# Kernel optimization log

Measured on AMD Instinct MI355X. Metric: run time of the kernel, lower is better.

Reference implementation:

```python
import jax, jax.numpy as jnp
import numpy as np

N, E = 10000, 320000
IN, H, C, ED = 256, 4, 64, 64
HC = H * C
EPS = 1e-5
NEG_SLOPE = 0.2


def setup_inputs() -> dict:
    key = jax.random.key(0)
    ks = jax.random.split(key, 12)
    g = lambda k, shape, fan: jax.random.normal(k, shape, jnp.float32) * (1.0 / np.sqrt(fan))
    return {
        "x": jax.random.normal(ks[0], (N, IN), jnp.float32),
        "edge_index": jax.random.randint(ks[1], (2, E), 0, N, jnp.int64),
        "edge_attr": jax.random.normal(ks[2], (E, ED), jnp.float32),
        "Wl": g(ks[3], (HC, IN), IN),   # lin_l weight (source)
        "bl": jnp.zeros((HC,), jnp.float32),
        "Wr": g(ks[4], (HC, IN), IN),   # lin_r weight (target)
        "br": jnp.zeros((HC,), jnp.float32),
        "We": g(ks[5], (HC, ED), ED),   # lin_edge weight (no bias)
        "att": g(ks[6], (H, C), C),
        "bias": jnp.zeros((HC,), jnp.float32),
        "gamma": jnp.ones((HC,), jnp.float32),
        "beta": jnp.zeros((HC,), jnp.float32),
    }


def reference(x, edge_index, edge_attr, Wl, bl, Wr, br, We, att, bias, gamma, beta):
    src, dst = edge_index[0], edge_index[1]
    # add_self_loops with fill_value='mean': loop edge_attr = mean of incoming attrs
    ones = jnp.ones((E,), jnp.float32)
    cnt = jax.ops.segment_sum(ones, dst, num_segments=N)              # [N]
    loop_attr = jax.ops.segment_sum(edge_attr, dst, num_segments=N) / jnp.maximum(cnt, 1.0)[:, None]
    node_ids = jnp.arange(N, dtype=src.dtype)
    src_f = jnp.concatenate([src, node_ids])                          # [E+N]
    dst_f = jnp.concatenate([dst, node_ids])
    ea = jnp.concatenate([edge_attr, loop_attr], axis=0)              # [E+N, ED]

    xl = (x @ Wl.T + bl).reshape(N, H, C)   # source-side projection
    xr = (x @ Wr.T + br).reshape(N, H, C)   # target-side projection
    ep = (ea @ We.T).reshape(-1, H, C)       # edge projection

    m = xl[src_f] + xr[dst_f] + ep                                    # [E+N, H, C]
    m = jnp.where(m >= 0, m, NEG_SLOPE * m)                           # leaky_relu(0.2)
    logits = jnp.einsum("ehc,hc->eh", m, att)                        # [E+N, H]

    # segment softmax over target node dst_f (every node has a self loop)
    mx = jax.ops.segment_max(logits, dst_f, num_segments=N)
    ex = jnp.exp(logits - mx[dst_f])
    den = jax.ops.segment_sum(ex, dst_f, num_segments=N)
    alpha = ex / den[dst_f]                                           # [E+N, H]

    out = jax.ops.segment_sum(xl[src_f] * alpha[:, :, None], dst_f, num_segments=N)
    h = out.reshape(N, HC) + bias

    # SiLU then LayerNorm, dropout is identity in eval
    h = h * jax.nn.sigmoid(h)
    mu = jnp.mean(h, axis=-1, keepdims=True)
    var = jnp.mean((h - mu) ** 2, axis=-1, keepdims=True)
    h = (h - mu) * jax.lax.rsqrt(var + EPS) * gamma + beta
    return h, alpha
```

## Files before the change

kernel.cpp:

```cpp
#include <hip/hip_runtime.h>

#define N_NODES 10000
#define N_EDGES 320000
#define NE_TOT  330000
#define NEG_SLOPE 0.2f
#define LN_EPS 1e-5f

#define OFF_CNT    0u
#define OFF_FILL   40000u
#define OFF_ROWPTR 80128u
#define OFF_EIDS   120320u
#define OFF_LATTR  1440512u
#define OFF_XLH    4000512u
#define OFF_XRH    9120512u
#define OFF_LOG    14240512u
#define OFF_WLF    19520512u
#define OFF_WRF    19651584u

typedef __bf16 bf16x8 __attribute__((ext_vector_type(8)));
typedef float  f32x4  __attribute__((ext_vector_type(4)));
typedef unsigned short us4 __attribute__((ext_vector_type(4)));

__device__ __forceinline__ float bf2f(unsigned short u) {
    union { unsigned int i; float f; } v;
    v.i = ((unsigned int)u) << 16;
    return v.f;
}
__device__ __forceinline__ unsigned short f2bf(float x) {
    __bf16 b = (__bf16)x;
    return __builtin_bit_cast(unsigned short, b);
}
__device__ __forceinline__ bf16x8 cvt8(const float* p) {
    float4 v0 = *reinterpret_cast<const float4*>(p);
    float4 v1 = *reinterpret_cast<const float4*>(p + 4);
    bf16x8 t;
    t[0] = (__bf16)v0.x; t[1] = (__bf16)v0.y; t[2] = (__bf16)v0.z; t[3] = (__bf16)v0.w;
    t[4] = (__bf16)v1.x; t[5] = (__bf16)v1.y; t[6] = (__bf16)v1.z; t[7] = (__bf16)v1.w;
    return t;
}

__global__ void k_count(const int* __restrict__ ei, int* __restrict__ cnt) {
    int e = blockIdx.x * blockDim.x + threadIdx.x;
    if (e < N_EDGES) atomicAdd(&cnt[ei[N_EDGES + e]], 1);
}

__global__ void k_scan(const int* __restrict__ cnt, int* __restrict__ row_ptr) {
    __shared__ int sums[1024];
    int t = threadIdx.x;
    const int CH = 10;
    int base = t * CH;
    int s = 0;
    for (int i = 0; i < CH; i++) {
        int n = base + i;
        if (n < N_NODES) s += cnt[n] + 1;
    }
    sums[t] = s;
    __syncthreads();
    for (int off = 1; off < 1024; off <<= 1) {
        int v = (t >= off) ? sums[t - off] : 0;
        __syncthreads();
        sums[t] += v;
        __syncthreads();
    }
    int run = (t == 0) ? 0 : sums[t - 1];
    for (int i = 0; i < CH; i++) {
        int n = base + i;
        if (n < N_NODES) { row_ptr[n] = run; run += cnt[n] + 1; }
    }
    if (t == 1023) row_ptr[N_NODES] = sums[1023];
}

__global__ void k_fill(const int* __restrict__ ei, const int* __restrict__ row_ptr,
                       int* __restrict__ fill, int* __restrict__ eids) {
    int e = blockIdx.x * blockDim.x + threadIdx.x;
    if (e >= NE_TOT) return;
    int d = (e < N_EDGES) ? ei[N_EDGES + e] : (e - N_EDGES);
    int pos = atomicAdd(&fill[d], 1);
    eids[row_ptr[d] + pos] = e;
}

__global__ void k_loop_attr(const float* __restrict__ edge_attr,
                            const int* __restrict__ row_ptr,
                            const int* __restrict__ eids,
                            const int* __restrict__ cnt,
                            float* __restrict__ lattr) {
    int node = (blockIdx.x << 2) + (threadIdx.x >> 6);
    int lane = threadIdx.x & 63;
    int b = row_ptr[node], en = row_ptr[node + 1];
    float s0 = 0.0f, s1 = 0.0f, s2 = 0.0f, s3 = 0.0f;
    int i = b;
    for (; i + 3 < en; i += 4) {
        int e0 = eids[i], e1 = eids[i + 1], e2 = eids[i + 2], e3 = eids[i + 3];
        int v0 = e0 < N_EDGES, v1 = e1 < N_EDGES, v2 = e2 < N_EDGES, v3 = e3 < N_EDGES;
        float a0 = edge_attr[(size_t)(v0 ? e0 : 0) * 64 + lane];
        float a1 = edge_attr[(size_t)(v1 ? e1 : 0) * 64 + lane];
        float a2 = edge_attr[(size_t)(v2 ? e2 : 0) * 64 + lane];
        float a3 = edge_attr[(size_t)(v3 ? e3 : 0) * 64 + lane];
        s0 += v0 ? a0 : 0.0f;
        s1 += v1 ? a1 : 0.0f;
        s2 += v2 ? a2 : 0.0f;
        s3 += v3 ? a3 : 0.0f;
    }
    for (; i < en; i++) {
        int e = eids[i];
        int v = e < N_EDGES;
        float a = edge_attr[(size_t)(v ? e : 0) * 64 + lane];
        s0 += v ? a : 0.0f;
    }
    float s = (s0 + s1) + (s2 + s3);
    float c = (float)cnt[node];
    lattr[node * 64 + lane] = s / fmaxf(c, 1.0f);
}

__global__ void k_prep_wfrag(const float* __restrict__ Wl,
                             const float* __restrict__ Wr,
                             unsigned short* __restrict__ wlf,
                             unsigned short* __restrict__ wrf) {
    int idx = blockIdx.x * 256 + threadIdx.x;
    if (idx >= 8192) return;
    int ln = idx & 63;
    int ts = (idx >> 6) & 7;
    int ct = idx >> 9;
    int c = ct * 16 + (ln & 15);
    int k0 = ts * 32 + (ln >> 4) * 8;
    *reinterpret_cast<bf16x8*>(wlf + (size_t)idx * 8) = cvt8(Wl + (size_t)c * 256 + k0);
    *reinterpret_cast<bf16x8*>(wrf + (size_t)idx * 8) = cvt8(Wr + (size_t)c * 256 + k0);
}

__global__ __launch_bounds__(256) void k_gemm_mfma(
        const float* __restrict__ x,
        const float* __restrict__ bl, const float* __restrict__ br,
        const unsigned short* __restrict__ wlf,
        const unsigned short* __restrict__ wrf,
        unsigned short* __restrict__ xlh,
        unsigned short* __restrict__ xrh) {
    __shared__ __bf16 xs[8 * 64 * 8];
    int tid = threadIdx.x;
    int nb = blockIdx.x * 16;

    for (int f = tid; f < 512; f += 256) {
        int t = f >> 6, ln = f & 63;
        int node = nb + (ln & 15);
        int k0 = t * 32 + (ln >> 4) * 8;
        *reinterpret_cast<bf16x8*>(&xs[f * 8]) = cvt8(x + (size_t)node * 256 + k0);
    }
    __syncthreads();

    int lane = tid & 63;
    int wv = tid >> 6;
    int quad = lane >> 4;
    int ln15 = lane & 15;

    bf16x8 bfr[8];
#pragma unroll
    for (int t = 0; t < 8; t++)
        bfr[t] = *reinterpret_cast<const bf16x8*>(&xs[(t * 64 + lane) * 8]);

    int node = nb + ln15;
#pragma unroll
    for (int ci = 0; ci < 4; ci++) {
        int ct = wv * 4 + ci;
        f32x4 accl, accr;
        accl[0] = accl[1] = accl[2] = accl[3] = 0.0f;
        accr[0] = accr[1] = accr[2] = accr[3] = 0.0f;
#pragma unroll
        for (int t = 0; t < 8; t++) {
            bf16x8 al = *reinterpret_cast<const bf16x8*>(
                wlf + ((size_t)(ct * 8 + t) * 64 + lane) * 8);
            accl = __builtin_amdgcn_mfma_f32_16x16x32_bf16(al, bfr[t], accl, 0, 0, 0);
        }
#pragma unroll
        for (int t = 0; t < 8; t++) {
            bf16x8 ar = *reinterpret_cast<const bf16x8*>(
                wrf + ((size_t)(ct * 8 + t) * 64 + lane) * 8);
            accr = __builtin_amdgcn_mfma_f32_16x16x32_bf16(ar, bfr[t], accr, 0, 0, 0);
        }
        int cbase = ct * 16 + quad * 4;
        float4 blv = *reinterpret_cast<const float4*>(bl + cbase);
        float4 brv = *reinterpret_cast<const float4*>(br + cbase);
        us4 ol, orr;
        ol[0] = f2bf(accl[0] + blv.x); ol[1] = f2bf(accl[1] + blv.y);
        ol[2] = f2bf(accl[2] + blv.z); ol[3] = f2bf(accl[3] + blv.w);
        orr[0] = f2bf(accr[0] + brv.x); orr[1] = f2bf(accr[1] + brv.y);
        orr[2] = f2bf(accr[2] + brv.z); orr[3] = f2bf(accr[3] + brv.w);
        *reinterpret_cast<us4*>(xlh + (size_t)node * 256 + cbase) = ol;
        *reinterpret_cast<us4*>(xrh + (size_t)node * 256 + cbase) = orr;
    }
}

__global__ __launch_bounds__(256) void k_logits_mfma(
        const int* __restrict__ ei,
        const int* __restrict__ eids,
        const float* __restrict__ edge_attr,
        const float* __restrict__ lattr,
        const unsigned short* __restrict__ xlh,
        const unsigned short* __restrict__ xrh,
        const float* __restrict__ We, const float* __restrict__ att,
        float* __restrict__ logits) {
    __shared__ __bf16 fb[32 * 64 * 8];
    __shared__ float att_s[256];
    int tid = threadIdx.x;

    for (int idx = tid; idx < 2048; idx += 256) {
        int f = idx >> 6, ls = idx & 63;
        int cb = f >> 1, step = f & 1;
        int c = cb * 16 + (ls & 15);
        int k = step * 32 + (ls >> 4) * 8;
        *reinterpret_cast<bf16x8*>(&fb[idx * 8]) = cvt8(We + (size_t)c * 64 + k);
    }
    if (tid < 64) {
        reinterpret_cast<float4*>(att_s)[tid] =
            reinterpret_cast<const float4*>(att)[tid];
    }
    __syncthreads();

    int lane = tid & 63;
    int wv = tid >> 6;
    int quad = lane >> 4;
    int ln15 = lane & 15;

    const int ntiles = NE_TOT / 16;
    for (int t = blockIdx.x * 4 + wv; t < ntiles; t += gridDim.x * 4) {
        int pos = t * 16 + ln15;
        int e = eids[pos];
        int s, d;
        const float* row;
        if (e < N_EDGES) {
            s = ei[e]; d = ei[N_EDGES + e];
            row = edge_attr + (size_t)e * 64;
        } else {
            s = e - N_EDGES; d = s;
            row = lattr + (size_t)(e - N_EDGES) * 64;
        }

        bf16x8 bfr[2];
#pragma unroll
        for (int step = 0; step < 2; step++)
            bfr[step] = cvt8(row + step * 32 + quad * 8);

        const unsigned short* xls = xlh + (size_t)s * 256;
        const unsigned short* xrd = xrh + (size_t)d * 256;

        float hsum[4] = {0.0f, 0.0f, 0.0f, 0.0f};
#pragma unroll 4
        for (int cb = 0; cb < 16; cb++) {
            f32x4 acc;
            acc[0] = acc[1] = acc[2] = acc[3] = 0.0f;
            bf16x8 a0 = *reinterpret_cast<const bf16x8*>(&fb[((cb * 2 + 0) * 64 + lane) * 8]);
            bf16x8 a1 = *reinterpret_cast<const bf16x8*>(&fb[((cb * 2 + 1) * 64 + lane) * 8]);
            acc = __builtin_amdgcn_mfma_f32_16x16x32_bf16(a0, bfr[0], acc, 0, 0, 0);
            acc = __builtin_amdgcn_mfma_f32_16x16x32_bf16(a1, bfr[1], acc, 0, 0, 0);

            int cbase = cb * 16 + quad * 4;
            us4 xa = *reinterpret_cast<const us4*>(xls + cbase);
            us4 xb = *reinterpret_cast<const us4*>(xrd + cbase);
            float4 at = *reinterpret_cast<const float4*>(&att_s[cbase]);
            const float* tp = reinterpret_cast<const float*>(&at);
            float hs = 0.0f;
#pragma unroll
            for (int r = 0; r < 4; r++) {
                float v = acc[r] + bf2f(xa[r]) + bf2f(xb[r]);
                v = (v >= 0.0f) ? v : NEG_SLOPE * v;
                hs = fmaf(v, tp[r], hs);
            }
            hsum[cb >> 2] += hs;
        }
#pragma unroll
        for (int hh = 0; hh < 4; hh++) {
            hsum[hh] += __shfl_xor(hsum[hh], 16, 64);
            hsum[hh] += __shfl_xor(hsum[hh], 32, 64);
        }
        if (quad == 0) {
            reinterpret_cast<float4*>(logits)[pos] =
                make_float4(hsum[0], hsum[1], hsum[2], hsum[3]);
        }
    }
}

__global__ void k_aggregate(const int* __restrict__ ei,
                            const int* __restrict__ row_ptr,
                            const int* __restrict__ eids,
                            const float* __restrict__ logits,
                            const unsigned short* __restrict__ xlh,
                            const float* __restrict__ bias,
                            const float* __restrict__ gamma,
                            const float* __restrict__ beta,
                            float* __restrict__ hout,
                            float* __restrict__ alpha_out) {
    int node = (blockIdx.x << 2) + (threadIdx.x >> 6);
    int lane = threadIdx.x & 63;
    int h = lane >> 4;
    int b = row_ptr[node], en = row_ptr[node + 1];

    float m0 = -INFINITY, m1 = -INFINITY, m2 = -INFINITY, m3 = -INFINITY;
    int i = b;
    for (; i + 3 < en; i += 4) {
        m0 = fmaxf(m0, logits[(i + 0) * 4 + h]);
        m1 = fmaxf(m1, logits[(i + 1) * 4 + h]);
        m2 = fmaxf(m2, logits[(i + 2) * 4 + h]);
        m3 = fmaxf(m3, logits[(i + 3) * 4 + h]);
    }
    for (; i < en; i++) m0 = fmaxf(m0, logits[i * 4 + h]);
    float mh = fmaxf(fmaxf(m0, m1), fmaxf(m2, m3));

    float d0 = 0.0f, d1 = 0.0f, d2 = 0.0f, d3 = 0.0f;
    i = b;
    for (; i + 3 < en; i += 4) {
        d0 += __expf(logits[(i + 0) * 4 + h] - mh);
        d1 += __expf(logits[(i + 1) * 4 + h] - mh);
        d2 += __expf(logits[(i + 2) * 4 + h] - mh);
        d3 += __expf(logits[(i + 3) * 4 + h] - mh);
    }
    for (; i < en; i++) d0 += __expf(logits[i * 4 + h] - mh);
    float rden = 1.0f / ((d0 + d1) + (d2 + d3));

    int c0 = lane * 4;
    float4 ac0; ac0.x = ac0.y = ac0.z = ac0.w = 0.0f;
    float4 ac1; ac1.x = ac1.y = ac1.z = ac1.w = 0.0f;
    float4 ac2; ac2.x = ac2.y = ac2.z = ac2.w = 0.0f;
    float4 ac3; ac3.x = ac3.y = ac3.z = ac3.w = 0.0f;
    i = b;
    for (; i + 3 < en; i += 4) {
        int e0 = eids[i], e1 = eids[i + 1], e2 = eids[i + 2], e3 = eids[i + 3];
        float al0 = __expf(logits[(i + 0) * 4 + h] - mh) * rden;
        float al1 = __expf(logits[(i + 1) * 4 + h] - mh) * rden;
        float al2 = __expf(logits[(i + 2) * 4 + h] - mh) * rden;
        float al3 = __expf(logits[(i + 3) * 4 + h] - mh) * rden;
        if ((lane & 15) == 0) {
            alpha_out[e0 * 4 + h] = al0;
            alpha_out[e1 * 4 + h] = al1;
            alpha_out[e2 * 4 + h] = al2;
            alpha_out[e3 * 4 + h] = al3;
        }
        int s0 = (e0 < N_EDGES) ? ei[e0] : (e0 - N_EDGES);
        int s1 = (e1 < N_EDGES) ? ei[e1] : (e1 - N_EDGES);
        int s2 = (e2 < N_EDGES) ? ei[e2] : (e2 - N_EDGES);
        int s3 = (e3 < N_EDGES) ? ei[e3] : (e3 - N_EDGES);
        us4 x0 = *reinterpret_cast<const us4*>(xlh + (size_t)s0 * 256 + c0);
        us4 x1 = *reinterpret_cast<const us4*>(xlh + (size_t)s1 * 256 + c0);
        us4 x2 = *reinterpret_cast<const us4*>(xlh + (size_t)s2 * 256 + c0);
        us4 x3 = *reinterpret_cast<const us4*>(xlh + (size_t)s3 * 256 + c0);
        ac0.x = fmaf(al0, bf2f(x0[0]), ac0.x); ac0.y = fmaf(al0, bf2f(x0[1]), ac0.y);
        ac0.z = fmaf(al0, bf2f(x0[2]), ac0.z); ac0.w = fmaf(al0, bf2f(x0[3]), ac0.w);
        ac1.x = fmaf(al1, bf2f(x1[0]), ac1.x); ac1.y = fmaf(al1, bf2f(x1[1]), ac1.y);
        ac1.z = fmaf(al1, bf2f(x1[2]), ac1.z); ac1.w = fmaf(al1, bf2f(x1[3]), ac1.w);
        ac2.x = fmaf(al2, bf2f(x2[0]), ac2.x); ac2.y = fmaf(al2, bf2f(x2[1]), ac2.y);
        ac2.z = fmaf(al2, bf2f(x2[2]), ac2.z); ac2.w = fmaf(al2, bf2f(x2[3]), ac2.w);
        ac3.x = fmaf(al3, bf2f(x3[0]), ac3.x); ac3.y = fmaf(al3, bf2f(x3[1]), ac3.y);
        ac3.z = fmaf(al3, bf2f(x3[2]), ac3.z); ac3.w = fmaf(al3, bf2f(x3[3]), ac3.w);
    }
    for (; i < en; i++) {
        int e = eids[i];
        float al = __expf(logits[i * 4 + h] - mh) * rden;
        if ((lane & 15) == 0) alpha_out[e * 4 + h] = al;
        int s = (e < N_EDGES) ? ei[e] : (e - N_EDGES);
        us4 xv = *reinterpret_cast<const us4*>(xlh + (size_t)s * 256 + c0);
        ac0.x = fmaf(al, bf2f(xv[0]), ac0.x); ac0.y = fmaf(al, bf2f(xv[1]), ac0.y);
        ac0.z = fmaf(al, bf2f(xv[2]), ac0.z); ac0.w = fmaf(al, bf2f(xv[3]), ac0.w);
    }
    float4 acc;
    acc.x = (ac0.x + ac1.x) + (ac2.x + ac3.x);
    acc.y = (ac0.y + ac1.y) + (ac2.y + ac3.y);
    acc.z = (ac0.z + ac1.z) + (ac2.z + ac3.z);
    acc.w = (ac0.w + ac1.w) + (ac2.w + ac3.w);

    const float4 b4 = reinterpret_cast<const float4*>(bias)[lane];
    float4 hv;
    hv.x = acc.x + b4.x; hv.y = acc.y + b4.y;
    hv.z = acc.z + b4.z; hv.w = acc.w + b4.w;
    hv.x = hv.x / (1.0f + __expf(-hv.x));
    hv.y = hv.y / (1.0f + __expf(-hv.y));
    hv.z = hv.z / (1.0f + __expf(-hv.z));
    hv.w = hv.w / (1.0f + __expf(-hv.w));
    float s1 = hv.x + hv.y + hv.z + hv.w;
    float s2 = hv.x * hv.x + hv.y * hv.y + hv.z * hv.z + hv.w * hv.w;
#pragma unroll
    for (int off = 1; off < 64; off <<= 1) {
        s1 += __shfl_xor(s1, off, 64);
        s2 += __shfl_xor(s2, off, 64);
    }
    float mu = s1 * (1.0f / 256.0f);
    float var = s2 * (1.0f / 256.0f) - mu * mu;
    float rs = rsqrtf(var + LN_EPS);
    const float4 g4 = reinterpret_cast<const float4*>(gamma)[lane];
    const float4 be4 = reinterpret_cast<const float4*>(beta)[lane];
    float4 o;
    o.x = (hv.x - mu) * rs * g4.x + be4.x;
    o.y = (hv.y - mu) * rs * g4.y + be4.y;
    o.z = (hv.z - mu) * rs * g4.z + be4.z;
    o.w = (hv.w - mu) * rs * g4.w + be4.w;
    reinterpret_cast<float4*>(hout)[node * 64 + lane] = o;
}

extern "C" void kernel_launch(void* const* d_in, const int* in_sizes, int n_in,
                              void* d_out, int out_size, void* d_ws, size_t ws_size,
                              hipStream_t stream) {
    (void)in_sizes; (void)n_in; (void)out_size; (void)ws_size;
    const float* x         = (const float*)d_in[0];
    const int*   ei        = (const int*)d_in[1];
    const float* edge_attr = (const float*)d_in[2];
    const float* Wl        = (const float*)d_in[3];
    const float* bl        = (const float*)d_in[4];
    const float* Wr        = (const float*)d_in[5];
    const float* br        = (const float*)d_in[6];
    const float* We        = (const float*)d_in[7];
    const float* att       = (const float*)d_in[8];
    const float* bias      = (const float*)d_in[9];
    const float* gamma     = (const float*)d_in[10];
    const float* beta      = (const float*)d_in[11];

    char* ws = (char*)d_ws;
    int*   cnt     = (int*)(ws + OFF_CNT);
    int*   fill    = (int*)(ws + OFF_FILL);
    int*   row_ptr = (int*)(ws + OFF_ROWPTR);
    int*   eids    = (int*)(ws + OFF_EIDS);
    float* lattr   = (float*)(ws + OFF_LATTR);
    unsigned short* xlh = (unsigned short*)(ws + OFF_XLH);
    unsigned short* xrh = (unsigned short*)(ws + OFF_XRH);
    float* logits  = (float*)(ws + OFF_LOG);
    unsigned short* wlf = (unsigned short*)(ws + OFF_WLF);
    unsigned short* wrf = (unsigned short*)(ws + OFF_WRF);

    float* hout      = (float*)d_out;
    float* alpha_out = (float*)d_out + N_NODES * 256;

    hipMemsetAsync(ws + OFF_CNT, 0, 2 * N_NODES * sizeof(int), stream);

    k_count<<<(N_EDGES + 255) / 256, 256, 0, stream>>>(ei, cnt);
    k_scan<<<1, 1024, 0, stream>>>(cnt, row_ptr);
    k_prep_wfrag<<<32, 256, 0, stream>>>(Wl, Wr, wlf, wrf);
    k_fill<<<(NE_TOT + 255) / 256, 256, 0, stream>>>(ei, row_ptr, fill, eids);
    k_gemm_mfma<<<N_NODES / 16, 256, 0, stream>>>(x, bl, br, wlf, wrf, xlh, xrh);
    k_loop_attr<<<N_NODES / 4, 256, 0, stream>>>(edge_attr, row_ptr, eids, cnt, lattr);
    k_logits_mfma<<<2579, 256, 0, stream>>>(ei, eids, edge_attr, lattr, xlh, xrh,
                                            We, att, logits);
    k_aggregate<<<N_NODES / 4, 256, 0, stream>>>(ei, row_ptr, eids, logits, xlh,
                                                 bias, gamma, beta, hout, alpha_out);
}
```

Before: 379.4 us.

## Store per-edge src/dst in CSR order and pre-permute edge attrs to bf16

During CSR fill, the source and destination of each edge are written in sorted order, along with an inverse permutation. When the workspace is large enough, edge attributes are scattered into CSR order as bf16 and the self-loop mean is computed in place. The logits kernel can then read src, dst and attributes contiguously instead of gathering through eids and ei. This adds a scatter pass and extra workspace traffic, and the self-loop mean is now averaged from bf16-rounded attributes.

```diff
diff --git a/kernel.cpp b/kernel.cpp
--- a/kernel.cpp
+++ b/kernel.cpp
@@ -9,17 +9,23 @@
 #define OFF_CNT    0u
 #define OFF_FILL   40000u
 #define OFF_ROWPTR 80128u
-#define OFF_EIDS   120320u
-#define OFF_LATTR  1440512u
-#define OFF_XLH    4000512u
-#define OFF_XRH    9120512u
-#define OFF_LOG    14240512u
-#define OFF_WLF    19520512u
-#define OFF_WRF    19651584u
+#define OFF_EIDS   120192u
+#define OFF_SRCS   1440192u
+#define OFF_DSTS   2760192u
+#define OFF_LATTR  4080192u
+#define OFF_XLH    6640192u
+#define OFF_XRH    11760192u
+#define OFF_LOG    16880192u
+#define OFF_WLF    22160192u
+#define OFF_WRF    22291264u
+#define OFF_INV    22422336u
+#define OFF_EAP    23742336u
+#define WS_NEED_A  65982336u
 
 typedef __bf16 bf16x8 __attribute__((ext_vector_type(8)));
 typedef float  f32x4  __attribute__((ext_vector_type(4)));
 typedef unsigned short us4 __attribute__((ext_vector_type(4)));
+typedef unsigned short us8 __attribute__((ext_vector_type(8)));
 
 __device__ __forceinline__ float bf2f(unsigned short u) {
     union { unsigned int i; float f; } v;
@@ -71,18 +77,54 @@
 }
 
 __global__ void k_fill(const int* __restrict__ ei, const int* __restrict__ row_ptr,
-                       int* __restrict__ fill, int* __restrict__ eids) {
+                       int* __restrict__ fill, int* __restrict__ eids,
+                       int* __restrict__ srcs, int* __restrict__ dsts,
+                       int* __restrict__ inv) {
     int e = blockIdx.x * blockDim.x + threadIdx.x;
     if (e >= NE_TOT) return;
-    int d = (e < N_EDGES) ? ei[N_EDGES + e] : (e - N_EDGES);
+    int s, d;
+    if (e < N_EDGES) { s = ei[e]; d = ei[N_EDGES + e]; }
+    else             { s = e - N_EDGES; d = s; }
     int pos = atomicAdd(&fill[d], 1);
-    eids[row_ptr[d] + pos] = e;
+    int p = row_ptr[d] + pos;
+    eids[p] = e;
+    srcs[p] = s;
+    dsts[p] = d;
+    inv[e] = p;
+}
+
+__global__ void k_perm_ea(const float* __restrict__ edge_attr,
+                          const int* __restrict__ inv,
+                          unsigned short* __restrict__ eap) {
+    int e = blockIdx.x * 4 + (threadIdx.x >> 6);
+    int lane = threadIdx.x & 63;
+    if (e >= N_EDGES) return;
+    float v = edge_attr[(size_t)e * 64 + lane];
+    eap[(size_t)inv[e] * 64 + lane] = f2bf(v);
+}
+
+__global__ void k_selfmean(const int* __restrict__ row_ptr,
+                           const int* __restrict__ eids,
+                           unsigned short* __restrict__ eap) {
+    int node = (blockIdx.x << 2) + (threadIdx.x >> 6);
+    int lane = threadIdx.x & 63;
+    int b = row_ptr[node], en = row_ptr[node + 1];
+    float s = 0.0f;
+    int selfpos = b;
+    for (int i = b; i < en; i++) {
+        int e = eids[i];
+        bool real = (e < N_EDGES);
+        unsigned short u = eap[(size_t)i * 64 + lane];
+        s += real ? bf2f(u) : 0.0f;
+        selfpos = real ? selfpos : i;
+    }
+    float c = (float)(en - b - 1);
+    eap[(size_t)selfpos * 64 + lane] = f2bf(s / fmaxf(c, 1.0f));
 }
 
 __global__ void k_loop_attr(const float* __restrict__ edge_attr,
                             const int* __restrict__ row_ptr,
                             const int* __restrict__ eids,
-                            const int* __restrict__ cnt,
                             float* __restrict__ lattr) {
     int node = (blockIdx.x << 2) + (threadIdx.x >> 6);
     int lane = threadIdx.x & 63;
@@ -108,7 +150,7 @@
         s0 += v ? a : 0.0f;
     }
     float s = (s0 + s1) + (s2 + s3);
-    float c = (float)cnt[node];
+    float c = (float)(en - b - 1);
     lattr[node * 64 + lane] = s / fmaxf(c, 1.0f);
 }
 
@@ -188,8 +230,10 @@
     }
 }
 
+template <bool USE_EAP>
 __global__ __launch_bounds__(256) void k_logits_mfma(
-        const int* __restrict__ ei,
+        const int* __restrict__ srcs, const int* __restrict__ dsts,
+        const unsigned short* __restrict__ eap,
         const int* __restrict__ eids,
         const float* __restrict__ edge_attr,
         const float* __restrict__ lattr,
@@ -222,21 +266,22 @@
     const int ntiles = NE_TOT / 16;
     for (int t = blockIdx.x * 4 + wv; t < ntiles; t += gridDim.x * 4) {
         int pos = t * 16 + ln15;
-        int e = eids[pos];
-        int s, d;
-        const float* row;
-        if (e < N_EDGES) {
-            s = ei[e]; d = ei[N_EDGES + e];
-            row = edge_attr + (size_t)e * 64;
+        int s = srcs[pos];
+        int d = dsts[pos];
+
+        bf16x8 bfr[2];
+        if (USE_EAP) {
+            const unsigned short* er = eap + (size_t)pos * 64 + quad * 8;
+            bfr[0] = __builtin_bit_cast(bf16x8, *reinterpret_cast<const us8*>(er));
+            bfr[1] = __builtin_bit_cast(bf16x8, *reinterpret_cast<const us8*>(er + 32));
         } else {
-            s = e - N_EDGES; d = s;
-            row = lattr + (size_t)(e - N_EDGES) * 64;
-        }
-
-        bf16x8 bfr[2];
-#pragma unroll
-        for (int step = 0; step < 2; step++)
-            bfr[step] = cvt8(row + step * 32 + quad * 8);
+            int e = eids[pos];
+            const float* row = (e < N_EDGES)
+                ? edge_attr + (size_t)e * 64
+                : lattr + (size_t)(e - N_EDGES) * 64;
+            bfr[0] = cvt8(row + quad * 8);
+            bfr[1] = cvt8(row + 32 + quad * 8);
+        }
 
         const unsigned short* xls = xlh + (size_t)s * 256;
         const unsigned short* xrd = xrh + (size_t)d * 256;
@@ -277,9 +322,9 @@
     }
 }
 
-__global__ void k_aggregate(const int* __restrict__ ei,
-                            const int* __restrict__ row_ptr,
+__global__ void k_aggregate(const int* __restrict__ row_ptr,
                             const int* __restrict__ eids,
+                            const int* __restrict__ srcs,
                             const float* __restrict__ logits,
                             const unsigned short* __restrict__ xlh,
                             const float* __restrict__ bias,
@@ -322,6 +367,7 @@
     i = b;
     for (; i + 3 < en; i += 4) {
         int e0 = eids[i], e1 = eids[i + 1], e2 = eids[i + 2], e3 = eids[i + 3];
+        int s0 = srcs[i], s1 = srcs[i + 1], s2 = srcs[i + 2], s3 = srcs[i + 3];
         float al0 = __expf(logits[(i + 0) * 4 + h] - mh) * rden;
         float al1 = __expf(logits[(i + 1) * 4 + h] - mh) * rden;
         float al2 = __expf(logits[(i + 2) * 4 + h] - mh) * rden;
@@ -332,10 +378,6 @@
             alpha_out[e2 * 4 + h] = al2;
             alpha_out[e3 * 4 + h] = al3;
         }
-        int s0 = (e0 < N_EDGES) ? ei[e0] : (e0 - N_EDGES);
-        int s1 = (e1 < N_EDGES) ? ei[e1] : (e1 - N_EDGES);
-        int s2 = (e2 < N_EDGES) ? ei[e2] : (e2 - N_EDGES);
-        int s3 = (e3 < N_EDGES) ? ei[e3] : (e3 - N_EDGES);
         us4 x0 = *reinterpret_cast<const us4*>(xlh + (size_t)s0 * 256 + c0);
         us4 x1 = *reinterpret_cast<const us4*>(xlh + (size_t)s1 * 256 + c0);
         us4 x2 = *reinterpret_cast<const us4*>(xlh + (size_t)s2 * 256 + c0);
@@ -351,9 +393,9 @@
     }
     for (; i < en; i++) {
         int e = eids[i];
+        int s = srcs[i];
         float al = __expf(logits[i * 4 + h] - mh) * rden;
         if ((lane & 15) == 0) alpha_out[e * 4 + h] = al;
-        int s = (e < N_EDGES) ? ei[e] : (e - N_EDGES);
         us4 xv = *reinterpret_cast<const us4*>(xlh + (size_t)s * 256 + c0);
         ac0.x = fmaf(al, bf2f(xv[0]), ac0.x); ac0.y = fmaf(al, bf2f(xv[1]), ac0.y);
         ac0.z = fmaf(al, bf2f(xv[2]), ac0.z); ac0.w = fmaf(al, bf2f(xv[3]), ac0.w);
@@ -395,7 +437,7 @@
 extern "C" void kernel_launch(void* const* d_in, const int* in_sizes, int n_in,
                               void* d_out, int out_size, void* d_ws, size_t ws_size,
                               hipStream_t stream) {
-    (void)in_sizes; (void)n_in; (void)out_size; (void)ws_size;
+    (void)in_sizes; (void)n_in; (void)out_size;
     const float* x         = (const float*)d_in[0];
     const int*   ei        = (const int*)d_in[1];
     const float* edge_attr = (const float*)d_in[2];
@@ -414,26 +456,42 @@
     int*   fill    = (int*)(ws + OFF_FILL);
     int*   row_ptr = (int*)(ws + OFF_ROWPTR);
     int*   eids    = (int*)(ws + OFF_EIDS);
+    int*   srcs    = (int*)(ws + OFF_SRCS);
+    int*   dsts    = (int*)(ws + OFF_DSTS);
     float* lattr   = (float*)(ws + OFF_LATTR);
     unsigned short* xlh = (unsigned short*)(ws + OFF_XLH);
     unsigned short* xrh = (unsigned short*)(ws + OFF_XRH);
     float* logits  = (float*)(ws + OFF_LOG);
     unsigned short* wlf = (unsigned short*)(ws + OFF_WLF);
     unsigned short* wrf = (unsigned short*)(ws + OFF_WRF);
+    int*   inv     = (int*)(ws + OFF_INV);
+    unsigned short* eap = (unsigned short*)(ws + OFF_EAP);
 
     float* hout      = (float*)d_out;
     float* alpha_out = (float*)d_out + N_NODES * 256;
+
+    const bool big = (ws_size >= (size_t)WS_NEED_A);
 
     hipMemsetAsync(ws + OFF_CNT, 0, 2 * N_NODES * sizeof(int), stream);
 
     k_count<<<(N_EDGES + 255) / 256, 256, 0, stream>>>(ei, cnt);
     k_scan<<<1, 1024, 0, stream>>>(cnt, row_ptr);
     k_prep_wfrag<<<32, 256, 0, stream>>>(Wl, Wr, wlf, wrf);
-    k_fill<<<(NE_TOT + 255) / 256, 256, 0, stream>>>(ei, row_ptr, fill, eids);
+    k_fill<<<(NE_TOT + 255) / 256, 256, 0, stream>>>(ei, row_ptr, fill, eids,
+                                                     srcs, dsts, inv);
     k_gemm_mfma<<<N_NODES / 16, 256, 0, stream>>>(x, bl, br, wlf, wrf, xlh, xrh);
-    k_loop_attr<<<N_NODES / 4, 256, 0, stream>>>(edge_attr, row_ptr, eids, cnt, lattr);
-    k_logits_mfma<<<2579, 256, 0, stream>>>(ei, eids, edge_attr, lattr, xlh, xrh,
-                                            We, att, logits);
-    k_aggregate<<<N_NODES / 4, 256, 0, stream>>>(ei, row_ptr, eids, logits, xlh,
+    if (big) {
+        k_perm_ea<<<N_EDGES / 4, 256, 0, stream>>>(edge_attr, inv, eap);
+        k_selfmean<<<N_NODES / 4, 256, 0, stream>>>(row_ptr, eids, eap);
+        k_logits_mfma<true><<<2579, 256, 0, stream>>>(srcs, dsts, eap, eids,
+                                                      edge_attr, lattr, xlh, xrh,
+                                                      We, att, logits);
+    } else {
+        k_loop_attr<<<N_NODES / 4, 256, 0, stream>>>(edge_attr, row_ptr, eids, lattr);
+        k_logits_mfma<false><<<2579, 256, 0, stream>>>(srcs, dsts, eap, eids,
+                                                       edge_attr, lattr, xlh, xrh,
+                                                       We, att, logits);
+    }
+    k_aggregate<<<N_NODES / 4, 256, 0, stream>>>(row_ptr, eids, srcs, logits, xlh,
                                                  bias, gamma, beta, hout, alpha_out);
 }
```

After: 422.5 us. +11.3%, slower.
